# Performance work log

Measured on AMD Instinct MI355X. Metric: run time of the kernel, lower is better.

The kernel has to match this reference:

```python
import jax, jax.numpy as jnp
import numpy as np

DIM = 2048
DIM_SEQ = 2048
HEADS = 4
BATCH = 4
LN_EPS = 1e-5  # torch nn.LayerNorm default


def setup_inputs() -> dict:
    key = jax.random.key(0)
    k1, k2 = jax.random.split(key)
    init_eps = 0.001 / DIM_SEQ
    x = jax.random.normal(k1, (BATCH, DIM_SEQ, DIM), dtype=jnp.float32)
    weight = jax.random.uniform(k2, (HEADS, DIM_SEQ, DIM_SEQ), dtype=jnp.float32,
                                minval=-init_eps, maxval=init_eps)
    bias = jnp.ones((HEADS, DIM_SEQ), dtype=jnp.float32)
    ln_gamma = jnp.ones((DIM // 2,), dtype=jnp.float32)
    ln_beta = jnp.zeros((DIM // 2,), dtype=jnp.float32)
    return {"x": x, "weight": weight, "bias": bias,
            "ln_gamma": ln_gamma, "ln_beta": ln_beta}


def _layernorm(x, gamma, beta):
    mu = jnp.mean(x, axis=-1, keepdims=True)
    var = jnp.mean(jnp.square(x - mu), axis=-1, keepdims=True)
    return (x - mu) * jax.lax.rsqrt(var + LN_EPS) * gamma + beta


def reference(x, weight, bias, ln_gamma, ln_beta):
    b, n, _ = x.shape
    h = HEADS
    res, gate = jnp.split(x, 2, axis=-1)          # each [b, n, dim/2]
    gate = _layernorm(gate, ln_gamma, ln_beta)
    w = weight[:, :n, :n]                          # [h, n, n]
    bi = bias[:, :n]                               # [h, n]
    # causal: zero strictly-upper triangle (output pos m attends n <= m)
    w = w * jnp.tril(jnp.ones((n, n), dtype=w.dtype))
    d = gate.shape[-1] // h
    gate = gate.reshape(b, n, h, d).transpose(0, 2, 1, 3)   # [b, h, n, d]
    gate = jnp.einsum('bhnd,hmn->bhmd', gate, w)
    gate = gate + bi[None, :, :, None]
    gate = gate.transpose(0, 2, 1, 3).reshape(b, n, h * d)  # [b, n, dim/2]
    return gate * res
```

## Files before the change

### kernel.cpp

```cpp
#include <hip/hip_runtime.h>
#include <hip/hip_bf16.h>


constexpr int Bb = 4;
constexpr int Nn = 2048;
constexpr int DX = 2048;
constexpr int GD = 1024;
constexpr int DH = 256;

typedef short short8v __attribute__((ext_vector_type(8)));
typedef float f32x4   __attribute__((ext_vector_type(4)));

static __device__ __forceinline__ short f2bf(float f) {
    return __builtin_bit_cast(short, __float2bfloat16(f));
}

static __device__ __forceinline__ void gll16(const void* g, void* l) {
    __builtin_amdgcn_global_load_lds(
        (const __attribute__((address_space(1))) void*)g,
        (__attribute__((address_space(3))) void*)l, 16, 0, 0);
}

__global__ __launch_bounds__(256) void ln_stats_kernel(const float* __restrict__ x,
                                                       float2* __restrict__ mr) {
    int t = threadIdx.x;
    int row = blockIdx.x * 4 + (t >> 6);
    int lane = t & 63;
    const float4* xr = reinterpret_cast<const float4*>(x + (size_t)row * DX + GD);
    float s = 0.f, ss = 0.f;
#pragma unroll
    for (int q = 0; q < 4; ++q) {
        float4 v = xr[q * 64 + lane];
        s  += v.x + v.y + v.z + v.w;
        ss += v.x*v.x + v.y*v.y + v.z*v.z + v.w*v.w;
    }
#pragma unroll
    for (int off = 32; off >= 1; off >>= 1) {
        s  += __shfl_down(s,  off, 64);
        ss += __shfl_down(ss, off, 64);
    }
    if (lane == 0) {
        float m   = s * (1.f / GD);
        float var = ss * (1.f / GD) - m * m;
        mr[row] = make_float2(m, rsqrtf(var + 1e-5f));
    }
}

__global__ __launch_bounds__(256) void wcvt_kernel(const float* __restrict__ w,
                                                   short* __restrict__ wt) {
    const int hm = blockIdx.x;
    const int kt = blockIdx.y;
    const int mt = hm & 15, h = hm >> 4;
    if (kt > 4 * mt + 3) return;
    const int t = threadIdx.x;
    const int m0 = mt * 128, n0 = kt * 32;
    short* tile = wt + ((size_t)hm * 64 + kt) * 4096;
#pragma unroll
    for (int j = 0; j < 2; ++j) {
        int s  = 2 * t + j;
        int r  = s >> 2;
        int k8 = (s & 3) ^ ((r >> 1) & 3);
        const float* src = w + (size_t)(h * Nn + m0 + r) * Nn + n0 + k8 * 8;
        float4 a = *reinterpret_cast<const float4*>(src);
        float4 c = *reinterpret_cast<const float4*>(src + 4);
        const int m = m0 + r, nb0 = n0 + k8 * 8;
        float av[8] = {a.x, a.y, a.z, a.w, c.x, c.y, c.z, c.w};
        short8v o;
#pragma unroll
        for (int e = 0; e < 8; ++e) o[e] = f2bf((nb0 + e) <= m ? av[e] : 0.f);
        *reinterpret_cast<short8v*>(tile + s * 8) = o;
    }
}

__global__ __launch_bounds__(256) void gcvt_kernel(const float* __restrict__ x,
                                                   const float* __restrict__ gamma,
                                                   const float* __restrict__ beta,
                                                   const float2* __restrict__ mr,
                                                   short* __restrict__ gt) {
    __shared__ short T[128 * 136];
    const int nb = blockIdx.x, cblk = blockIdx.y, b = blockIdx.z;
    const int t = threadIdx.x;
    const int n0b = nb * 128, c0 = cblk * 128;
    const int c4 = (t & 31) * 4, rg = t >> 5;

    const float* src = x + (size_t)b * Nn * DX + GD + c0 + c4;
    float4 gm = *reinterpret_cast<const float4*>(gamma + c0 + c4);
    float4 bt = *reinterpret_cast<const float4*>(beta  + c0 + c4);
    const float2* mrb = mr + b * Nn + n0b;

#pragma unroll
    for (int i = 0; i < 16; ++i) {
        int n = i * 8 + rg;
        float2 ms = mrb[n];
        float4 v  = *reinterpret_cast<const float4*>(src + (size_t)(n0b + n) * DX);
        T[(c4 + 0) * 136 + n] = f2bf((v.x - ms.x) * ms.y * gm.x + bt.x);
        T[(c4 + 1) * 136 + n] = f2bf((v.y - ms.x) * ms.y * gm.y + bt.y);
        T[(c4 + 2) * 136 + n] = f2bf((v.z - ms.x) * ms.y * gm.z + bt.z);
        T[(c4 + 3) * 136 + n] = f2bf((v.w - ms.x) * ms.y * gm.w + bt.w);
    }
    __syncthreads();
#pragma unroll
    for (int kq = 0; kq < 4; ++kq) {
        short* tile = gt + ((size_t)(b * 8 + cblk) * 64 + (nb * 4 + kq)) * 4096;
#pragma unroll
        for (int j = 0; j < 2; ++j) {
            int s  = 2 * t + j;
            int c  = s >> 2;
            int n8 = (s & 3) ^ ((c >> 1) & 3);
            short8v v = *reinterpret_cast<const short8v*>(&T[c * 136 + kq * 32 + n8 * 8]);
            *reinterpret_cast<short8v*>(tile + s * 8) = v;
        }
    }
}

__global__ __launch_bounds__(256, 3) void sgu_mfma_kernel(
    const float* __restrict__ x, const short* __restrict__ wt,
    const short* __restrict__ gt, const float* __restrict__ bias,
    float* __restrict__ out)
{
    __shared__ __align__(16) short WS[2][4096];
    __shared__ __align__(16) short GS[2][4096];

    const int t  = threadIdx.x;
    const int bx = blockIdx.x;
    const int dc = bx & 1;
    const int h  = (bx >> 1) & 3;
    const int b  = bx >> 3;
    const int y  = blockIdx.y;
    const int mt = (y < 8) ? (15 - 2 * y) : ((y - 8) * 2);
    const int m0 = mt * 128;
    const int cb = h * DH + dc * 128;
    const int nk = 4 * mt + 4;

    const int lane = t & 63;
    const int wv = t >> 6;
    const int wm = wv >> 1, wc = wv & 1;
    const int g  = lane >> 4;
    const int lr = lane & 15;

    const char* wtb = (const char*)wt + ((size_t)(h * 16 + mt) * 64) * 8192;
    const char* gtb = (const char*)gt + ((size_t)(b * 8 + h * 2 + dc) * 64) * 8192;
    const int soff = wv * 2048 + lane * 16;

    f32x4 acc[4][4] = {};

    auto STAGE = [&](int buf, int kt) {
        const char* ws = wtb + (size_t)kt * 8192 + soff;
        const char* gs = gtb + (size_t)kt * 8192 + soff;
        short* wd = &WS[buf][wv * 1024];
        short* gd = &GS[buf][wv * 1024];
        gll16(ws,        wd);
        gll16(ws + 1024, wd + 512);
        gll16(gs,        gd);
        gll16(gs + 1024, gd + 512);
    };

    auto COMPUTE = [&](int buf) {
        const char* wl = (const char*)&WS[buf][0];
        const char* gl = (const char*)&GS[buf][0];
        short8v af[4], bf[4];
#pragma unroll
        for (int fi = 0; fi < 4; ++fi) {
            int row = wm * 64 + fi * 16 + lr;
            unsigned off = (unsigned)(row * 64 + g * 16);
            off ^= ((unsigned)(row >> 1) & 3u) << 4;
            af[fi] = *reinterpret_cast<const short8v*>(wl + off);
        }
#pragma unroll
        for (int fj = 0; fj < 4; ++fj) {
            int c = wc * 64 + fj * 16 + lr;
            unsigned off = (unsigned)(c * 64 + g * 16);
            off ^= ((unsigned)(c >> 1) & 3u) << 4;
            bf[fj] = *reinterpret_cast<const short8v*>(gl + off);
        }
#pragma unroll
        for (int fi = 0; fi < 4; ++fi)
#pragma unroll
            for (int fj = 0; fj < 4; ++fj)
                acc[fi][fj] = __builtin_amdgcn_mfma_f32_16x16x32_bf16(
                    af[fi], bf[fj], acc[fi][fj], 0, 0, 0);
    };

    STAGE(0, 0);
    __syncthreads();
    int cur = 0;
    for (int kt = 0; kt < nk; ++kt) {
        if (kt + 1 < nk) STAGE(cur ^ 1, kt + 1);
        COMPUTE(cur);
        __syncthreads();
        cur ^= 1;
    }

    const float* xb = x + (size_t)b * Nn * DX;
#pragma unroll
    for (int fi = 0; fi < 4; ++fi) {
#pragma unroll
        for (int r = 0; r < 4; ++r) {
            int m = m0 + wm * 64 + fi * 16 + g * 4 + r;
            float bv = bias[h * Nn + m];
            const float* resrow = xb + (size_t)m * DX + cb;
            float* orow = out + ((size_t)b * Nn + m) * GD + cb;
#pragma unroll
            for (int fj = 0; fj < 4; ++fj) {
                int c = wc * 64 + fj * 16 + lr;
                orow[c] = (acc[fi][fj][r] + bv) * resrow[c];
            }
        }
    }
}

extern "C" void kernel_launch(void* const* d_in, const int* in_sizes, int n_in,
                              void* d_out, int out_size, void* d_ws, size_t ws_size,
                              hipStream_t stream) {
    const float* x     = (const float*)d_in[0];
    const float* w     = (const float*)d_in[1];
    const float* bias  = (const float*)d_in[2];
    const float* gamma = (const float*)d_in[3];
    const float* beta  = (const float*)d_in[4];
    float* out = (float*)d_out;

    const size_t MR_BYTES = 64 * 1024;
    const size_t GT_BYTES = (size_t)16 * 1024 * 1024;
    const size_t WT_BYTES = (size_t)32 * 1024 * 1024;
    if (ws_size < MR_BYTES + GT_BYTES + WT_BYTES) return;

    float2* mrw = (float2*)d_ws;
    short*  gtw = (short*)((char*)d_ws + MR_BYTES);
    short*  wtw = (short*)((char*)d_ws + MR_BYTES + GT_BYTES);

    ln_stats_kernel<<<Bb * Nn / 4, 256, 0, stream>>>(x, mrw);
    gcvt_kernel<<<dim3(16, 8, Bb), 256, 0, stream>>>(x, gamma, beta, mrw, gtw);
    wcvt_kernel<<<dim3(64, 64), 256, 0, stream>>>(w, wtw);
    sgu_mfma_kernel<<<dim3(32, 16), 256, 0, stream>>>(x, wtw, gtw, bias, out);
}
```

Baseline: 217.6 us.

## Halve MFMA output tile width and remap blocks for XCD-aware causal balancing

The main GEMM kernel now computes 128x64 output tiles instead of 128x128, doubling the grid to 1024 blocks, halving the gate LDS buffer and accumulator count, and raising the occupancy hint to 4 blocks per CU. Block indices are remapped so each group of 128 consecutive blocks shares one pair of complementary causal row tiles, which balances triangular work and groups weight-tile reuse per XCD. This targets load imbalance and low occupancy. In exchange each weight tile is loaded twice as often, and arithmetic intensity per block drops.

```diff
diff --git a/kernel.cpp b/kernel.cpp
--- a/kernel.cpp
+++ b/kernel.cpp
@@ -113,23 +113,25 @@
     }
 }
 
-__global__ __launch_bounds__(256, 3) void sgu_mfma_kernel(
+__global__ __launch_bounds__(256, 4) void sgu_mfma_kernel(
     const float* __restrict__ x, const short* __restrict__ wt,
     const short* __restrict__ gt, const float* __restrict__ bias,
     float* __restrict__ out)
 {
     __shared__ __align__(16) short WS[2][4096];
-    __shared__ __align__(16) short GS[2][4096];
+    __shared__ __align__(16) short GS[2][2048];
 
     const int t  = threadIdx.x;
-    const int bx = blockIdx.x;
-    const int dc = bx & 1;
-    const int h  = (bx >> 1) & 3;
-    const int b  = bx >> 3;
-    const int y  = blockIdx.y;
-    const int mt = (y < 8) ? (15 - 2 * y) : ((y - 8) * 2);
+    const int id = blockIdx.x;
+    const int xcd  = id >> 7;
+    const int half = (id >> 6) & 1;
+    const int xc   = id & 63;
+    const int mt   = half ? xcd : 15 - xcd;
+    const int dcq  = xc & 3;
+    const int h    = (xc >> 2) & 3;
+    const int b    = xc >> 4;
     const int m0 = mt * 128;
-    const int cb = h * DH + dc * 128;
+    const int cb = h * DH + dcq * 64;
     const int nk = 4 * mt + 4;
 
     const int lane = t & 63;
@@ -139,26 +141,27 @@
     const int lr = lane & 15;
 
     const char* wtb = (const char*)wt + ((size_t)(h * 16 + mt) * 64) * 8192;
-    const char* gtb = (const char*)gt + ((size_t)(b * 8 + h * 2 + dc) * 64) * 8192;
-    const int soff = wv * 2048 + lane * 16;
-
-    f32x4 acc[4][4] = {};
+    const char* gtb = (const char*)gt
+        + ((size_t)(b * 8 + h * 2 + (dcq >> 1)) * 64) * 8192 + (dcq & 1) * 4096;
+    const int wsoff = wv * 2048 + lane * 16;
+    const int gsoff = wv * 1024 + lane * 16;
+
+    f32x4 acc[4][2] = {};
 
     auto STAGE = [&](int buf, int kt) {
-        const char* ws = wtb + (size_t)kt * 8192 + soff;
-        const char* gs = gtb + (size_t)kt * 8192 + soff;
+        const char* ws = wtb + (size_t)kt * 8192 + wsoff;
+        const char* gs = gtb + (size_t)kt * 8192 + gsoff;
         short* wd = &WS[buf][wv * 1024];
-        short* gd = &GS[buf][wv * 1024];
+        short* gd = &GS[buf][wv * 512];
         gll16(ws,        wd);
         gll16(ws + 1024, wd + 512);
         gll16(gs,        gd);
-        gll16(gs + 1024, gd + 512);
     };
 
     auto COMPUTE = [&](int buf) {
         const char* wl = (const char*)&WS[buf][0];
         const char* gl = (const char*)&GS[buf][0];
-        short8v af[4], bf[4];
+        short8v af[4], bf[2];
 #pragma unroll
         for (int fi = 0; fi < 4; ++fi) {
             int row = wm * 64 + fi * 16 + lr;
@@ -167,16 +170,16 @@
             af[fi] = *reinterpret_cast<const short8v*>(wl + off);
         }
 #pragma unroll
-        for (int fj = 0; fj < 4; ++fj) {
-            int c = wc * 64 + fj * 16 + lr;
-            unsigned off = (unsigned)(c * 64 + g * 16);
-            off ^= ((unsigned)(c >> 1) & 3u) << 4;
+        for (int fj = 0; fj < 2; ++fj) {
+            int rp = wc * 32 + fj * 16 + lr;
+            unsigned off = (unsigned)(rp * 64 + g * 16);
+            off ^= ((unsigned)(rp >> 1) & 3u) << 4;
             bf[fj] = *reinterpret_cast<const short8v*>(gl + off);
         }
 #pragma unroll
         for (int fi = 0; fi < 4; ++fi)
 #pragma unroll
-            for (int fj = 0; fj < 4; ++fj)
+            for (int fj = 0; fj < 2; ++fj)
                 acc[fi][fj] = __builtin_amdgcn_mfma_f32_16x16x32_bf16(
                     af[fi], bf[fj], acc[fi][fj], 0, 0, 0);
     };
@@ -201,8 +204,8 @@
             const float* resrow = xb + (size_t)m * DX + cb;
             float* orow = out + ((size_t)b * Nn + m) * GD + cb;
 #pragma unroll
-            for (int fj = 0; fj < 4; ++fj) {
-                int c = wc * 64 + fj * 16 + lr;
+            for (int fj = 0; fj < 2; ++fj) {
+                int c = wc * 32 + fj * 16 + lr;
                 orow[c] = (acc[fi][fj][r] + bv) * resrow[c];
             }
         }
@@ -231,5 +234,5 @@
     ln_stats_kernel<<<Bb * Nn / 4, 256, 0, stream>>>(x, mrw);
     gcvt_kernel<<<dim3(16, 8, Bb), 256, 0, stream>>>(x, gamma, beta, mrw, gtw);
     wcvt_kernel<<<dim3(64, 64), 256, 0, stream>>>(w, wtw);
-    sgu_mfma_kernel<<<dim3(32, 16), 256, 0, stream>>>(x, wtw, gtw, bias, out);
-}
+    sgu_mfma_kernel<<<1024, 256, 0, stream>>>(x, wtw, gtw, bias, out);
+}
```

Result: no change. 214.9 us (-1.2%).
